# Kernel optimization log

Hardware: AMD Instinct MI355X
Metric: run time of the kernel (lower is better)

Reference implementation:

```python
import jax, jax.numpy as jnp
import numpy as np

HIDDEN = 2560
NH = 32            # num_attention_heads
HD = HIDDEN // NH  # head_size = 80
RD = 32            # rotary_dim = int(0.4 * 80)
THETA = 10000.0
B, S = 2, 2048


def _rope_cos_sin(position_ids):
    # neox-style partial RoPE over the first RD dims of each head
    inv_freq = 1.0 / (THETA ** (jnp.arange(0, RD, 2, dtype=jnp.float32) / RD))  # [RD/2]
    freqs = position_ids.astype(jnp.float32)[..., None] * inv_freq  # [B,S,RD/2]
    return jnp.cos(freqs), jnp.sin(freqs)


def _apply_rope(x, cos, sin):
    # x: [B,S,NH,HD]; rotate first RD dims (neox: halves are paired)
    rot, rest = x[..., :RD], x[..., RD:]
    x1, x2 = rot[..., : RD // 2], rot[..., RD // 2:]
    c = cos[:, :, None, :]
    s = sin[:, :, None, :]
    o1 = x1 * c - x2 * s
    o2 = x2 * c + x1 * s
    return jnp.concatenate([o1, o2, rest], axis=-1)


def setup_inputs() -> dict:
    key = jax.random.key(0)
    ks = jax.random.split(key, 6)
    position_ids = jnp.tile(jnp.arange(S, dtype=jnp.int64)[None, :], (B, 1))
    return {
        "position_ids": position_ids,
        "hidden_states": jax.random.normal(ks[0], (B, S, HIDDEN), dtype=jnp.float32),
        "w_qkv": jax.random.normal(ks[1], (HIDDEN, 3 * HIDDEN), dtype=jnp.float32) * 0.02,
        "b_qkv": jax.random.normal(ks[2], (3 * HIDDEN,), dtype=jnp.float32) * 0.02,
        "w_dense": jax.random.normal(ks[3], (HIDDEN, HIDDEN), dtype=jnp.float32) * 0.02,
        "b_dense": jax.random.normal(ks[4], (HIDDEN,), dtype=jnp.float32) * 0.02,
    }


def reference(position_ids, hidden_states, w_qkv, b_qkv, w_dense, b_dense):
    scale = HD ** -0.5
    qkv = hidden_states @ w_qkv + b_qkv          # [B,S,3*HIDDEN]
    q, k, v = jnp.split(qkv, 3, axis=-1)
    q = q.reshape(B, S, NH, HD)
    k = k.reshape(B, S, NH, HD)
    v = v.reshape(B, S, NH, HD)
    cos, sin = _rope_cos_sin(position_ids)
    q = _apply_rope(q, cos, sin)
    k = _apply_rope(k, cos, sin)
    scores = jnp.einsum("bqhd,bkhd->bhqk", q, k) * scale  # [B,NH,S,S]
    causal = jnp.tril(jnp.ones((S, S), dtype=bool))
    scores = jnp.where(causal[None, None], scores, jnp.finfo(scores.dtype).min)
    probs = jax.nn.softmax(scores, axis=-1)
    attn = jnp.einsum("bhqk,bkhd->bqhd", probs, v).reshape(B, S, HIDDEN)
    return attn @ w_dense + b_dense
```

## Files before the change

kernel.cpp:

```cpp
#include <hip/hip_runtime.h>

#define S_LEN 2048
#define NHEAD 32
#define HD 80
#define DPAD 96
#define HIDDEN 2560
#define QKV_N 7680

typedef __attribute__((ext_vector_type(8))) short bf16x8;
typedef __attribute__((ext_vector_type(8))) unsigned short u16x8;
typedef __attribute__((ext_vector_type(4))) float f32x4;

__device__ __forceinline__ unsigned short f2bf(float f) {
  unsigned int u = __float_as_uint(f);
  u += 0x7fffu + ((u >> 16) & 1u);
  return (unsigned short)(u >> 16);
}
__device__ __forceinline__ float bf2f(unsigned short h) {
  return __uint_as_float(((unsigned int)h) << 16);
}

__device__ __forceinline__ void gload16(const void* g, void* l) {
  __builtin_amdgcn_global_load_lds((const __attribute__((address_space(1))) void*)g,
                                   (__attribute__((address_space(3))) void*)l, 16, 0, 0);
}

__global__ __launch_bounds__(256) void k_cvt(const float* __restrict__ in,
                                             unsigned short* __restrict__ out, int n4) {
  int i = blockIdx.x * 256 + threadIdx.x;
  if (i >= n4) return;
  float4 v = reinterpret_cast<const float4*>(in)[i];
  ushort4 o;
  o.x = f2bf(v.x); o.y = f2bf(v.y); o.z = f2bf(v.z); o.w = f2bf(v.w);
  reinterpret_cast<ushort4*>(out)[i] = o;
}

__global__ __launch_bounds__(256) void k_transpose_bf16(const float* __restrict__ in,
                                                        unsigned short* __restrict__ out,
                                                        int R, int C) {
  __shared__ float tile[64][65];
  int tc = blockIdx.x * 64, tr = blockIdx.y * 64;
  for (int i = threadIdx.x; i < 64 * 64; i += 256) {
    int r = i >> 6, c = i & 63;
    tile[r][c] = in[(size_t)(tr + r) * C + (tc + c)];
  }
  __syncthreads();
  for (int i = threadIdx.x; i < 64 * 64; i += 256) {
    int r = i >> 6, c = i & 63;
    out[(size_t)(tc + r) * R + (tr + c)] = f2bf(tile[c][r]);
  }
}

template <int BM>
__global__ __launch_bounds__(BM / 32 * 64, 2)
void k_gemm_t(const unsigned short* __restrict__ A,
              const unsigned short* __restrict__ Bt,
              const float* __restrict__ bias,
              unsigned short* __restrict__ Cbf,
              float* __restrict__ Cf,
              int M, int N, int K, int out_f32) {
  constexpr int NW = BM / 32;
  constexpr int NCW = NW / 2;
  constexpr int MF = BM / 32;
  constexpr int TE = BM * 32;
  __shared__ unsigned short sA[4][TE];
  __shared__ unsigned short sB[4][TE];
  const int nbn = N / BM;
  const int nwg = (M / BM) * nbn;
  int wg = blockIdx.x;
  const int cpx = nwg >> 3;
  wg = (wg & 7) * cpx + (wg >> 3);
  const int bm = wg / nbn, bn = wg - bm * nbn;
  const int tid = threadIdx.x;
  const int lane = tid & 63, wave = tid >> 6;
  const int wr = wave / NCW, wc = wave % NCW;
  const int lc = lane & 15, lr = lane >> 4;

  const int sub = (lane & 7) ^ (lane >> 3);
  const int rstage = wave * 16 + ((lane >> 3) << 1) + (sub >> 2);
  const int cstage = (sub & 3) * 8;
  const unsigned short* Agp = A + (size_t)(bm * BM + rstage) * K + cstage;
  const unsigned short* Bgp = Bt + (size_t)(bn * BM + rstage) * K + cstage;
  const size_t halfoff = (size_t)(BM / 2) * K;

  const int loff = ((lc >> 1) << 7) + (((((lc & 1) << 2) | lr) ^ (lc >> 1)) << 4);

  f32x4 acc[MF][4];
  const f32x4 zero = {0.f, 0.f, 0.f, 0.f};
#pragma unroll
  for (int m = 0; m < MF; ++m)
#pragma unroll
    for (int n = 0; n < 4; ++n) acc[m][n] = zero;

  auto stage = [&](int buf, int t) {
    gload16(Agp + t * 32, &sA[buf][wave * 512]);
    gload16(Agp + halfoff + t * 32, &sA[buf][BM * 16 + wave * 512]);
    gload16(Bgp + t * 32, &sB[buf][wave * 512]);
    gload16(Bgp + halfoff + t * 32, &sB[buf][BM * 16 + wave * 512]);
  };

  const int NT = K >> 5;
#pragma unroll
  for (int t = 0; t < 3; ++t) stage(t, t);

  const int nj = NT >> 2;
  for (int j = 0; j < nj; ++j) {
#pragma unroll
    for (int to = 0; to < 4; ++to) {
      const int t = (j << 2) + to;
      if (t < NT - 2)       asm volatile("s_waitcnt vmcnt(8)" ::: "memory");
      else if (t == NT - 2) asm volatile("s_waitcnt vmcnt(4)" ::: "memory");
      else                  asm volatile("s_waitcnt vmcnt(0)" ::: "memory");
      __builtin_amdgcn_s_barrier();
      asm volatile("" ::: "memory");
      __builtin_amdgcn_sched_barrier(0);

      const char* bufA = (const char*)&sA[to][0];
      const char* bufB = (const char*)&sB[to][0];
      bf16x8 bfr[4], af[MF];
#pragma unroll
      for (int ni = 0; ni < 4; ++ni)
        bfr[ni] = *(const bf16x8*)(bufB + ((wc * 64 + ni * 16) << 6) + loff);
#pragma unroll
      for (int mi = 0; mi < MF; ++mi)
        af[mi] = *(const bf16x8*)(bufA + ((wr * (BM / 2) + mi * 16) << 6) + loff);

      if (t + 3 < NT) stage((to + 3) & 3, t + 3);

      __builtin_amdgcn_s_setprio(1);
#pragma unroll
      for (int mi = 0; mi < MF; ++mi)
#pragma unroll
        for (int ni = 0; ni < 4; ++ni)
          acc[mi][ni] = __builtin_amdgcn_mfma_f32_16x16x32_bf16(af[mi], bfr[ni], acc[mi][ni], 0, 0, 0);
      __builtin_amdgcn_s_setprio(0);
    }
  }

  const int rowb = bm * BM + wr * (BM / 2);
  const int colb = bn * BM + wc * 64;
#pragma unroll
  for (int ni = 0; ni < 4; ++ni) {
    const int col = colb + ni * 16 + lc;
    const float bv = bias[col];
#pragma unroll
    for (int mf = 0; mf < MF; ++mf) {
#pragma unroll
      for (int jj = 0; jj < 4; ++jj) {
        const int row = rowb + mf * 16 + lr * 4 + jj;
        const float v = acc[mf][ni][jj] + bv;
        if (out_f32) Cf[(size_t)row * N + col] = v;
        else Cbf[(size_t)row * N + col] = f2bf(v);
      }
    }
  }
}

__global__ __launch_bounds__(256) void k_rope(const unsigned short* __restrict__ qkv,
                                              unsigned short* __restrict__ Qw,
                                              unsigned short* __restrict__ Kw,
                                              unsigned short* __restrict__ Vt) {
  const int blk = blockIdx.x;
  const int sc = blk & 31;
  const int bh = blk >> 5;
  const int b = bh >> 5, h = bh & 31;
  const int s0 = sc * 64;
  __shared__ float cs0[64][16], sn0[64][16];
  __shared__ unsigned short vbuf[64][82];
  const int tid = threadIdx.x;
  for (int i = tid; i < 64 * 16; i += 256) {
    int sl = i >> 4, fi = i & 15;
    float ang = (float)(s0 + sl) * __expf(-(float)fi * 0.575646273248511421f);
    cs0[sl][fi] = cosf(ang);
    sn0[sl][fi] = sinf(ang);
  }
  __syncthreads();
  const size_t row0 = (size_t)(b * S_LEN + s0) * QKV_N;
  const size_t obase = ((size_t)bh * S_LEN + s0) * DPAD;
  for (int i = tid; i < 64 * DPAD; i += 256) {
    int sl = i / DPAD, d = i - sl * DPAD;
    float qv = 0.f, kv = 0.f;
    if (d < HD) {
      const unsigned short* rp = qkv + row0 + (size_t)sl * QKV_N + h * HD;
      float q = bf2f(rp[d]), k = bf2f(rp[HIDDEN + d]);
      if (d < 16) {
        float c = cs0[sl][d], s = sn0[sl][d];
        float q2 = bf2f(rp[d + 16]), k2 = bf2f(rp[HIDDEN + d + 16]);
        qv = q * c - q2 * s;
        kv = k * c - k2 * s;
      } else if (d < 32) {
        float c = cs0[sl][d - 16], s = sn0[sl][d - 16];
        float q1 = bf2f(rp[d - 16]), k1 = bf2f(rp[HIDDEN + d - 16]);
        qv = q * c + q1 * s;
        kv = k * c + k1 * s;
      } else {
        qv = q; kv = k;
      }
    }
    Qw[obase + (size_t)sl * DPAD + d] = f2bf(qv * 0.111803398874989485f);
    Kw[obase + (size_t)sl * DPAD + d] = f2bf(kv);
  }
  for (int i = tid; i < 64 * HD; i += 256) {
    int sl = i / HD, d = i - sl * HD;
    vbuf[sl][d] = qkv[row0 + (size_t)sl * QKV_N + 2 * HIDDEN + h * HD + d];
  }
  __syncthreads();
  const size_t vtb = (size_t)bh * DPAD * S_LEN + s0;
  for (int i = tid; i < DPAD * 64; i += 256) {
    int d = i >> 6, sl = i & 63;
    Vt[vtb + (size_t)d * S_LEN + sl] = (d < HD) ? vbuf[sl][d] : (unsigned short)0;
  }
}

__global__ __launch_bounds__(256, 2) void k_attn(const unsigned short* __restrict__ Qw,
                                                 const unsigned short* __restrict__ Kw,
                                                 const unsigned short* __restrict__ Vt,
                                                 unsigned short* __restrict__ O) {
  __shared__ unsigned short sK[2][64 * 104];
  __shared__ unsigned short sV[2][80 * 72];
  __shared__ unsigned short sP[4][16 * 72];
  const int p = blockIdx.x;
  const int bh = blockIdx.y;
  const int b = bh >> 5, h = bh & 31;
  const int tid = threadIdx.x;
  const int wave = tid >> 6, lane = tid & 63;
  const int lr = lane >> 4, lc = lane & 15;
  unsigned short* Pw = &sP[wave][0];

  const unsigned short* Kh = Kw + (size_t)bh * S_LEN * DPAD;
  const unsigned short* Vh = Vt + (size_t)bh * DPAD * S_LEN;
  const unsigned short* Qh = Qw + (size_t)bh * S_LEN * DPAD;

  const int kr = tid >> 2, kc = (tid & 3) * 24;
  const int vr = tid >> 3, vc = (tid & 7) * 8;

  u16x8 kst0, kst1, kst2, vst0, vst1, vst2;
  auto gload = [&](int t) {
    const unsigned short* Kg = Kh + ((size_t)(t * 64 + kr)) * DPAD + kc;
    kst0 = *(const u16x8*)(Kg);
    kst1 = *(const u16x8*)(Kg + 8);
    kst2 = *(const u16x8*)(Kg + 16);
    const unsigned short* Vg = Vh + (size_t)vr * S_LEN + t * 64 + vc;
    vst0 = *(const u16x8*)(Vg);
    vst1 = *(const u16x8*)(Vg + 32 * S_LEN);
    if (tid < 128) vst2 = *(const u16x8*)(Vg + (size_t)64 * S_LEN);
  };
  auto swrite = [&](int buf) {
    *(u16x8*)&sK[buf][kr * 104 + kc] = kst0;
    *(u16x8*)&sK[buf][kr * 104 + kc + 8] = kst1;
    *(u16x8*)&sK[buf][kr * 104 + kc + 16] = kst2;
    *(u16x8*)&sV[buf][vr * 72 + vc] = vst0;
    *(u16x8*)&sV[buf][(vr + 32) * 72 + vc] = vst1;
    if (tid < 128) *(u16x8*)&sV[buf][(vr + 64) * 72 + vc] = vst2;
  };

  const f32x4 zero = {0.f, 0.f, 0.f, 0.f};

#pragma unroll 1
  for (int qi = 0; qi < 2; ++qi) {
    const int qt = qi ? (15 - p) : p;
    const int nt = 2 * qt + 2;
    const int wbase = qt * 128 + wave * 32;

    bf16x8 qf[2][3];
#pragma unroll
    for (int m = 0; m < 2; ++m)
#pragma unroll
      for (int ks = 0; ks < 3; ++ks)
        qf[m][ks] = *(const bf16x8*)&Qh[(size_t)(wbase + m * 16 + lc) * DPAD + ks * 32 + lr * 8];

    f32x4 oacc[2][5];
#pragma unroll
    for (int m = 0; m < 2; ++m)
#pragma unroll
      for (int n = 0; n < 5; ++n) oacc[m][n] = zero;
    float mrun[2] = {-1e30f, -1e30f}, lrun[2] = {0.f, 0.f};

    gload(0);
    __syncthreads();
    swrite(0);
    int cur = 0;

#pragma unroll 1
    for (int t = 0; t < nt; ++t) {
      __syncthreads();
      if (t + 1 < nt) gload(t + 1);
      const int ktb = t * 64;
      const bool act0 = ktb <= wbase + 15;
      const bool act1 = ktb <= wbase + 31;
      if (act1) {
        const unsigned short* Kc = sK[cur];
        const unsigned short* Vc = sV[cur];
        f32x4 sf[2][4];
#pragma unroll
        for (int n = 0; n < 4; ++n) {
          sf[0][n] = zero; sf[1][n] = zero;
#pragma unroll
          for (int ks = 0; ks < 3; ++ks) {
            bf16x8 kf = *(const bf16x8*)&Kc[(n * 16 + lc) * 104 + ks * 32 + lr * 8];
            if (act0) sf[0][n] = __builtin_amdgcn_mfma_f32_16x16x32_bf16(kf, qf[0][ks], sf[0][n], 0, 0, 0);
            sf[1][n] = __builtin_amdgcn_mfma_f32_16x16x32_bf16(kf, qf[1][ks], sf[1][n], 0, 0, 0);
          }
        }
        bf16x8 vf[5][2];
#pragma unroll
        for (int n = 0; n < 5; ++n)
#pragma unroll
          for (int ks = 0; ks < 2; ++ks)
            vf[n][ks] = *(const bf16x8*)&Vc[(n * 16 + lc) * 72 + ks * 32 + lr * 8];
#pragma unroll
        for (int m = 0; m < 2; ++m) {
          if (m == 0 && !act0) continue;
          const int qrow0 = wbase + m * 16;
          if (ktb + 63 > qrow0) {
#pragma unroll
            for (int n = 0; n < 4; ++n)
#pragma unroll
              for (int j = 0; j < 4; ++j)
                if (ktb + n * 16 + lr * 4 + j > qrow0 + lc) sf[m][n][j] = -1e30f;
          }
          float t0 = sf[m][0][0];
#pragma unroll
          for (int n = 0; n < 4; ++n)
#pragma unroll
            for (int j = 0; j < 4; ++j) t0 = fmaxf(t0, sf[m][n][j]);
          t0 = fmaxf(t0, __shfl_xor(t0, 16));
          t0 = fmaxf(t0, __shfl_xor(t0, 32));
          const float nm = fmaxf(mrun[m], t0);
          const float corrq = __expf(mrun[m] - nm);
          mrun[m] = nm;
          float ps = 0.f;
#pragma unroll
          for (int n = 0; n < 4; ++n)
#pragma unroll
            for (int j = 0; j < 4; ++j) {
              float e = __expf(sf[m][n][j] - nm);
              sf[m][n][j] = e;
              ps += e;
            }
          ps += __shfl_xor(ps, 16);
          ps += __shfl_xor(ps, 32);
          lrun[m] = lrun[m] * corrq + ps;
          float cj[4];
#pragma unroll
          for (int j = 0; j < 4; ++j) cj[j] = __shfl(corrq, lr * 4 + j, 16);
#pragma unroll
          for (int n = 0; n < 5; ++n)
#pragma unroll
            for (int j = 0; j < 4; ++j) oacc[m][n][j] *= cj[j];
#pragma unroll
          for (int n = 0; n < 4; ++n) {
            unsigned lo = (unsigned)f2bf(sf[m][n][0]) | ((unsigned)f2bf(sf[m][n][1]) << 16);
            unsigned hi = (unsigned)f2bf(sf[m][n][2]) | ((unsigned)f2bf(sf[m][n][3]) << 16);
            uint2 u; u.x = lo; u.y = hi;
            *(uint2*)&Pw[lc * 72 + n * 16 + lr * 4] = u;
          }
          asm volatile("" ::: "memory");
          bf16x8 pa0 = *(const bf16x8*)&Pw[lc * 72 + lr * 8];
          bf16x8 pa1 = *(const bf16x8*)&Pw[lc * 72 + 32 + lr * 8];
#pragma unroll
          for (int n = 0; n < 5; ++n) {
            oacc[m][n] = __builtin_amdgcn_mfma_f32_16x16x32_bf16(pa0, vf[n][0], oacc[m][n], 0, 0, 0);
            oacc[m][n] = __builtin_amdgcn_mfma_f32_16x16x32_bf16(pa1, vf[n][1], oacc[m][n], 0, 0, 0);
          }
          asm volatile("" ::: "memory");
        }
      }
      if (t + 1 < nt) swrite(cur ^ 1);
      cur ^= 1;
    }

#pragma unroll
    for (int m = 0; m < 2; ++m) {
      float linv[4];
#pragma unroll
      for (int j = 0; j < 4; ++j) {
        float lj = __shfl(lrun[m], lr * 4 + j, 16);
        linv[j] = 1.f / lj;
      }
      const int q0 = wbase + m * 16 + lr * 4;
#pragma unroll
      for (int n = 0; n < 5; ++n) {
        const int d = n * 16 + lc;
#pragma unroll
        for (int j = 0; j < 4; ++j)
          O[((size_t)(b * S_LEN) + q0 + j) * HIDDEN + h * HD + d] = f2bf(oacc[m][n][j] * linv[j]);
      }
    }
  }
}

extern "C" void kernel_launch(void* const* d_in, const int* in_sizes, int n_in,
                              void* d_out, int out_size, void* d_ws, size_t ws_size,
                              hipStream_t stream) {
  (void)in_sizes; (void)n_in; (void)out_size; (void)ws_size;
  const float* hidden  = (const float*)d_in[1];
  const float* w_qkv   = (const float*)d_in[2];
  const float* b_qkv   = (const float*)d_in[3];
  const float* w_dense = (const float*)d_in[4];
  const float* b_dense = (const float*)d_in[5];
  char* ws = (char*)d_ws;
  unsigned short* Abf   = (unsigned short*)(ws + 0);
  unsigned short* Wqkvt = (unsigned short*)(ws + 20971520);
  unsigned short* Wdt   = (unsigned short*)(ws + 60293120);
  unsigned short* QKVb  = (unsigned short*)(ws + 73400320);
  unsigned short* Qw    = (unsigned short*)(ws + 136314880);
  unsigned short* Kw    = (unsigned short*)(ws + 161480704);
  unsigned short* Vt    = (unsigned short*)(ws + 186646528);
  unsigned short* Obf   = (unsigned short*)(ws + 211812352);

  k_cvt<<<10240, 256, 0, stream>>>(hidden, Abf, 2621440);
  k_transpose_bf16<<<dim3(120, 40), 256, 0, stream>>>(w_qkv, Wqkvt, 2560, 7680);
  k_transpose_bf16<<<dim3(40, 40), 256, 0, stream>>>(w_dense, Wdt, 2560, 2560);
  k_gemm_t<256><<<480, 512, 0, stream>>>(Abf, Wqkvt, b_qkv, QKVb, nullptr, 4096, 7680, 2560, 0);
  k_rope<<<2048, 256, 0, stream>>>(QKVb, Qw, Kw, Vt);
  k_attn<<<dim3(8, 64), 256, 0, stream>>>(Qw, Kw, Vt, Obf);
  k_gemm_t<128><<<640, 256, 0, stream>>>(Obf, Wdt, b_dense, nullptr, (float*)d_out, 4096, 2560, 2560, 1);
}
```

Baseline: 445.0 us.

## Add dedicated 256x256 QKV GEMM with K=64 double-buffered ping-pong pipeline

Replaces the generic templated GEMM for the QKV projection with a specialized kernel that stages 64-wide K tiles in two LDS buffers via direct global-to-LDS loads. Each iteration is split into four MFMA phases interleaved with loads of the next tiles, using barriers and s_setprio to overlap memory with compute. It also adds XCD-aware workgroup remapping and XOR-swizzled LDS layout. This trades more barriers and hand scheduling for better latency hiding; correctness depends on the manual vmcnt accounting.

```diff
diff --git a/kernel.cpp b/kernel.cpp
--- a/kernel.cpp
+++ b/kernel.cpp
@@ -48,6 +48,158 @@
   for (int i = threadIdx.x; i < 64 * 64; i += 256) {
     int r = i >> 6, c = i & 63;
     out[(size_t)(tc + r) * R + (tr + c)] = f2bf(tile[c][r]);
+  }
+}
+
+__global__ __launch_bounds__(512, 2)
+void k_gemm1(const unsigned short* __restrict__ A,
+             const unsigned short* __restrict__ Bt,
+             const float* __restrict__ bias,
+             unsigned short* __restrict__ Cbf,
+             int M, int N, int K) {
+  __shared__ unsigned short sA[2][16384];
+  __shared__ unsigned short sB[2][16384];
+  const int nbn = N >> 8;
+  const int nwg = (M >> 8) * nbn;
+  int wg = blockIdx.x;
+  const int cpx = nwg >> 3;
+  wg = (wg & 7) * cpx + (wg >> 3);
+  const int bm = wg / nbn, bn = wg - bm * nbn;
+  const int tid = threadIdx.x;
+  const int lane = tid & 63, wave = tid >> 6;
+  const int wr = wave >> 2, wc = wave & 3;
+  const int lc = lane & 15, lr = lane >> 4;
+
+  const int srow = tid >> 2;
+  const int schunk = (tid & 3) ^ (srow & 3);
+  const unsigned short* sa0 = A + (size_t)(bm * 256 + srow) * K + schunk * 8;
+  const unsigned short* sa1 = sa0 + (size_t)128 * K;
+  const unsigned short* sb0 = Bt + (size_t)(bn * 256 + srow) * K + schunk * 8;
+  const unsigned short* sb1 = sb0 + (size_t)128 * K;
+
+  auto stageA = [&](int bb, int ks, int koff) {
+    gload16(sa0 + koff, &sA[bb][ks * 8192 + tid * 8]);
+    gload16(sa1 + koff, &sA[bb][ks * 8192 + 4096 + tid * 8]);
+  };
+  auto stageB = [&](int bb, int ks, int koff) {
+    gload16(sb0 + koff, &sB[bb][ks * 8192 + tid * 8]);
+    gload16(sb1 + koff, &sB[bb][ks * 8192 + 4096 + tid * 8]);
+  };
+
+  const int rslot = (lr ^ (lc & 3)) * 8;
+
+  f32x4 acc[8][4];
+  const f32x4 zero = {0.f, 0.f, 0.f, 0.f};
+#pragma unroll
+  for (int m = 0; m < 8; ++m)
+#pragma unroll
+    for (int n = 0; n < 4; ++n) acc[m][n] = zero;
+
+  const int NT = K >> 6;
+
+  stageA(0, 0, 0);
+  stageB(0, 0, 0);
+  stageA(0, 1, 32);
+  stageB(0, 1, 32);
+  stageA(1, 0, 64);
+  stageB(1, 0, 64);
+  asm volatile("s_waitcnt vmcnt(4)" ::: "memory");
+  __builtin_amdgcn_s_barrier();
+
+  bf16x8 af[4], bf[4];
+  for (int t = 0; t < NT; ++t) {
+    const int b = t & 1, ob = b ^ 1;
+    const bool st1 = (t + 1) < NT, st2 = (t + 2) < NT;
+    const unsigned short* cA = &sA[b][0];
+    const unsigned short* cB = &sB[b][0];
+
+#pragma unroll
+    for (int nf = 0; nf < 4; ++nf)
+      bf[nf] = *(const bf16x8*)&cB[(wc * 64 + nf * 16 + lc) * 32 + rslot];
+#pragma unroll
+    for (int mf = 0; mf < 4; ++mf)
+      af[mf] = *(const bf16x8*)&cA[(wr * 128 + mf * 16 + lc) * 32 + rslot];
+    if (st1) stageA(ob, 1, (t + 1) * 64 + 32);
+    __builtin_amdgcn_s_barrier();
+    asm volatile("s_waitcnt lgkmcnt(0)" ::: "memory");
+    __builtin_amdgcn_sched_barrier(0);
+    __builtin_amdgcn_s_setprio(1);
+#pragma unroll
+    for (int mf = 0; mf < 4; ++mf)
+#pragma unroll
+      for (int nf = 0; nf < 4; ++nf)
+        acc[mf][nf] = __builtin_amdgcn_mfma_f32_16x16x32_bf16(af[mf], bf[nf], acc[mf][nf], 0, 0, 0);
+    __builtin_amdgcn_s_setprio(0);
+    __builtin_amdgcn_s_barrier();
+
+#pragma unroll
+    for (int mf = 0; mf < 4; ++mf)
+      af[mf] = *(const bf16x8*)&cA[(wr * 128 + (mf + 4) * 16 + lc) * 32 + rslot];
+    if (st1) stageB(ob, 1, (t + 1) * 64 + 32);
+    __builtin_amdgcn_s_barrier();
+    asm volatile("s_waitcnt lgkmcnt(0)" ::: "memory");
+    __builtin_amdgcn_sched_barrier(0);
+    __builtin_amdgcn_s_setprio(1);
+#pragma unroll
+    for (int mf = 0; mf < 4; ++mf)
+#pragma unroll
+      for (int nf = 0; nf < 4; ++nf)
+        acc[mf + 4][nf] = __builtin_amdgcn_mfma_f32_16x16x32_bf16(af[mf], bf[nf], acc[mf + 4][nf], 0, 0, 0);
+    __builtin_amdgcn_s_setprio(0);
+    __builtin_amdgcn_s_barrier();
+
+#pragma unroll
+    for (int nf = 0; nf < 4; ++nf)
+      bf[nf] = *(const bf16x8*)&cB[8192 + (wc * 64 + nf * 16 + lc) * 32 + rslot];
+#pragma unroll
+    for (int mf = 0; mf < 4; ++mf)
+      af[mf] = *(const bf16x8*)&cA[8192 + (wr * 128 + mf * 16 + lc) * 32 + rslot];
+    if (st2) stageB(b, 0, (t + 2) * 64);
+    __builtin_amdgcn_s_barrier();
+    asm volatile("s_waitcnt lgkmcnt(0)" ::: "memory");
+    __builtin_amdgcn_sched_barrier(0);
+    __builtin_amdgcn_s_setprio(1);
+#pragma unroll
+    for (int mf = 0; mf < 4; ++mf)
+#pragma unroll
+      for (int nf = 0; nf < 4; ++nf)
+        acc[mf][nf] = __builtin_amdgcn_mfma_f32_16x16x32_bf16(af[mf], bf[nf], acc[mf][nf], 0, 0, 0);
+    __builtin_amdgcn_s_setprio(0);
+    __builtin_amdgcn_s_barrier();
+
+#pragma unroll
+    for (int mf = 0; mf < 4; ++mf)
+      af[mf] = *(const bf16x8*)&cA[8192 + (wr * 128 + (mf + 4) * 16 + lc) * 32 + rslot];
+    if (st2) stageA(b, 0, (t + 2) * 64);
+    __builtin_amdgcn_s_barrier();
+    asm volatile("s_waitcnt lgkmcnt(0)" ::: "memory");
+    __builtin_amdgcn_sched_barrier(0);
+    __builtin_amdgcn_s_setprio(1);
+#pragma unroll
+    for (int mf = 0; mf < 4; ++mf)
+#pragma unroll
+      for (int nf = 0; nf < 4; ++nf)
+        acc[mf + 4][nf] = __builtin_amdgcn_mfma_f32_16x16x32_bf16(af[mf], bf[nf], acc[mf + 4][nf], 0, 0, 0);
+    __builtin_amdgcn_s_setprio(0);
+    if (st2)      asm volatile("s_waitcnt vmcnt(4)" ::: "memory");
+    else          asm volatile("s_waitcnt vmcnt(0)" ::: "memory");
+    __builtin_amdgcn_s_barrier();
+  }
+
+  const int rowb = bm * 256 + wr * 128;
+  const int colb = bn * 256 + wc * 64;
+#pragma unroll
+  for (int nf = 0; nf < 4; ++nf) {
+    const int col = colb + nf * 16 + lc;
+    const float bv = bias[col];
+#pragma unroll
+    for (int mf = 0; mf < 8; ++mf) {
+#pragma unroll
+      for (int jj = 0; jj < 4; ++jj) {
+        const int row = rowb + mf * 16 + lr * 4 + jj;
+        Cbf[(size_t)row * N + col] = f2bf(acc[mf][nf][jj] + bv);
+      }
+    }
   }
 }
 
@@ -412,7 +564,7 @@
   k_cvt<<<10240, 256, 0, stream>>>(hidden, Abf, 2621440);
   k_transpose_bf16<<<dim3(120, 40), 256, 0, stream>>>(w_qkv, Wqkvt, 2560, 7680);
   k_transpose_bf16<<<dim3(40, 40), 256, 0, stream>>>(w_dense, Wdt, 2560, 2560);
-  k_gemm_t<256><<<480, 512, 0, stream>>>(Abf, Wqkvt, b_qkv, QKVb, nullptr, 4096, 7680, 2560, 0);
+  k_gemm1<<<480, 512, 0, stream>>>(Abf, Wqkvt, b_qkv, QKVb, 4096, 7680, 2560);
   k_rope<<<2048, 256, 0, stream>>>(QKVb, Qw, Kw, Vt);
   k_attn<<<dim3(8, 64), 256, 0, stream>>>(Qw, Kw, Vt, Obf);
   k_gemm_t<128><<<640, 256, 0, stream>>>(Obf, Wdt, b_dense, nullptr, (float*)d_out, 4096, 2560, 2560, 1);
```

After: 453.6 us. No clear change (+1.9%).

## Software-pipeline LDS fragment reads in GEMM and shrink QKV GEMM tile

Applied to the files above, without the earlier changes.

Restructures the GEMM main loop to double-buffer register fragments: fragments for the next K-step are read from LDS while MFMAs run on the current ones, with one barrier per step placed after compute. The waitcnt logic is simplified to match. The QKV projection also switches from 256-wide tiles with 512 threads to 128-wide tiles with 1920 workgroups, giving more blocks but less operand reuse per tile. The extra fragment registers may raise register pressure and lower occupancy.

```diff
diff --git a/kernel.cpp b/kernel.cpp
--- a/kernel.cpp
+++ b/kernel.cpp
@@ -53,7 +53,7 @@
 
 template <int BM>
 __global__ __launch_bounds__(BM / 32 * 64, 2)
-void k_gemm_t(const unsigned short* __restrict__ A,
+void k_gemm_p(const unsigned short* __restrict__ A,
               const unsigned short* __restrict__ Bt,
               const float* __restrict__ bias,
               unsigned short* __restrict__ Cbf,
@@ -98,42 +98,61 @@
     gload16(Bgp + t * 32, &sB[buf][wave * 512]);
     gload16(Bgp + halfoff + t * 32, &sB[buf][BM * 16 + wave * 512]);
   };
+  auto rdfrags = [&](int buf, bf16x8 (&af)[MF], bf16x8 (&bf)[4]) {
+    const char* bufA = (const char*)&sA[buf][0];
+    const char* bufB = (const char*)&sB[buf][0];
+#pragma unroll
+    for (int ni = 0; ni < 4; ++ni)
+      bf[ni] = *(const bf16x8*)(bufB + ((wc * 64 + ni * 16) << 6) + loff);
+#pragma unroll
+    for (int mi = 0; mi < MF; ++mi)
+      af[mi] = *(const bf16x8*)(bufA + ((wr * (BM / 2) + mi * 16) << 6) + loff);
+  };
 
   const int NT = K >> 5;
-#pragma unroll
-  for (int t = 0; t < 3; ++t) stage(t, t);
-
-  const int nj = NT >> 2;
-  for (int j = 0; j < nj; ++j) {
-#pragma unroll
-    for (int to = 0; to < 4; ++to) {
-      const int t = (j << 2) + to;
-      if (t < NT - 2)       asm volatile("s_waitcnt vmcnt(8)" ::: "memory");
-      else if (t == NT - 2) asm volatile("s_waitcnt vmcnt(4)" ::: "memory");
-      else                  asm volatile("s_waitcnt vmcnt(0)" ::: "memory");
+
+  stage(0, 0);
+  stage(1, 1);
+  stage(2, 2);
+  asm volatile("s_waitcnt vmcnt(4)" ::: "memory");
+  __builtin_amdgcn_s_barrier();
+  __builtin_amdgcn_sched_barrier(0);
+
+  bf16x8 afX[MF], bfX[4], afY[MF], bfY[4];
+  rdfrags(0, afX, bfX);
+
+  for (int tt = 0; tt < NT; tt += 2) {
+    {
+      const int t = tt;
+      if (t + 1 < NT) rdfrags((t + 1) & 3, afY, bfY);
+      if (t + 3 < NT) stage((t + 3) & 3, t + 3);
+      __builtin_amdgcn_s_setprio(1);
+#pragma unroll
+      for (int mi = 0; mi < MF; ++mi)
+#pragma unroll
+        for (int ni = 0; ni < 4; ++ni)
+          acc[mi][ni] = __builtin_amdgcn_mfma_f32_16x16x32_bf16(afX[mi], bfX[ni], acc[mi][ni], 0, 0, 0);
+      __builtin_amdgcn_s_setprio(0);
+      if (t + 3 < NT) asm volatile("s_waitcnt vmcnt(4)" ::: "memory");
+      else            asm volatile("s_waitcnt vmcnt(0)" ::: "memory");
       __builtin_amdgcn_s_barrier();
-      asm volatile("" ::: "memory");
       __builtin_amdgcn_sched_barrier(0);
-
-      const char* bufA = (const char*)&sA[to][0];
-      const char* bufB = (const char*)&sB[to][0];
-      bf16x8 bfr[4], af[MF];
-#pragma unroll
-      for (int ni = 0; ni < 4; ++ni)
-        bfr[ni] = *(const bf16x8*)(bufB + ((wc * 64 + ni * 16) << 6) + loff);
+    }
+    {
+      const int t = tt + 1;
+      if (t + 1 < NT) rdfrags((t + 1) & 3, afX, bfX);
+      if (t + 3 < NT) stage((t + 3) & 3, t + 3);
+      __builtin_amdgcn_s_setprio(1);
 #pragma unroll
       for (int mi = 0; mi < MF; ++mi)
-        af[mi] = *(const bf16x8*)(bufA + ((wr * (BM / 2) + mi * 16) << 6) + loff);
-
-      if (t + 3 < NT) stage((to + 3) & 3, t + 3);
-
-      __builtin_amdgcn_s_setprio(1);
-#pragma unroll
-      for (int mi = 0; mi < MF; ++mi)
 #pragma unroll
         for (int ni = 0; ni < 4; ++ni)
-          acc[mi][ni] = __builtin_amdgcn_mfma_f32_16x16x32_bf16(af[mi], bfr[ni], acc[mi][ni], 0, 0, 0);
+          acc[mi][ni] = __builtin_amdgcn_mfma_f32_16x16x32_bf16(afY[mi], bfY[ni], acc[mi][ni], 0, 0, 0);
       __builtin_amdgcn_s_setprio(0);
+      if (t + 3 < NT) asm volatile("s_waitcnt vmcnt(4)" ::: "memory");
+      else            asm volatile("s_waitcnt vmcnt(0)" ::: "memory");
+      __builtin_amdgcn_s_barrier();
+      __builtin_amdgcn_sched_barrier(0);
     }
   }
 
@@ -412,8 +431,8 @@
   k_cvt<<<10240, 256, 0, stream>>>(hidden, Abf, 2621440);
   k_transpose_bf16<<<dim3(120, 40), 256, 0, stream>>>(w_qkv, Wqkvt, 2560, 7680);
   k_transpose_bf16<<<dim3(40, 40), 256, 0, stream>>>(w_dense, Wdt, 2560, 2560);
-  k_gemm_t<256><<<480, 512, 0, stream>>>(Abf, Wqkvt, b_qkv, QKVb, nullptr, 4096, 7680, 2560, 0);
+  k_gemm_p<128><<<1920, 256, 0, stream>>>(Abf, Wqkvt, b_qkv, QKVb, nullptr, 4096, 7680, 2560, 0);
   k_rope<<<2048, 256, 0, stream>>>(QKVb, Qw, Kw, Vt);
   k_attn<<<dim3(8, 64), 256, 0, stream>>>(Qw, Kw, Vt, Obf);
-  k_gemm_t<128><<<640, 256, 0, stream>>>(Obf, Wdt, b_dense, nullptr, (float*)d_out, 4096, 2560, 2560, 1);
-}
+  k_gemm_p<128><<<640, 256, 0, stream>>>(Obf, Wdt, b_dense, nullptr, (float*)d_out, 4096, 2560, 2560, 1);
+}
```

After: 528.7 us. 18.8% more time.
